# Performance work log

Measured on AMD Instinct MI355X. Metric: run time of the kernel, lower is better.

The kernel has to match this reference:

```python
import math
import jax, jax.numpy as jnp
import numpy as np

D_SCALES = 4  # MSGAD d parameter


def calc_thetas(d):
    # Numeric replication of calculate_theta2 (beta-wavelet polynomial coeffs).
    # p_i(x) = (x/2)^i (1 - x/2)^(d-i) / (2 * Beta(i+1, d+1-i)); keep the d
    # lowest-order coefficients (constant .. x^{d-1}), matching the original.
    thetas = []
    for i in range(d):
        beta = math.factorial(i) * math.factorial(d - i) / math.factorial(d + 1)
        p = (np.poly1d([0.5, 0.0]) ** i) * (np.poly1d([-0.5, 1.0]) ** (d - i)) / (2.0 * beta)
        c = p.coeffs  # highest degree first, length d+1
        thetas.append([float(c[d - j]) for j in range(d)])
    return thetas

THETAS = calc_thetas(D_SCALES)


def setup_inputs() -> dict:
    key = jax.random.key(0)
    k1, k2, k3, k4 = jax.random.split(key, 4)
    N, E, IN, H = 8192, 262144, 256, 128
    in_feat = jax.random.normal(k1, (N, IN), dtype=jnp.float32)
    W = jax.random.normal(k2, (IN, H), dtype=jnp.float32) * 0.05
    b = jnp.zeros((H,), dtype=jnp.float32)
    src = jax.random.randint(k3, (E,), 0, N, dtype=jnp.int32)
    dst = jax.random.randint(k4, (E,), 0, N, dtype=jnp.int32)
    return {"in_feat": in_feat, "W": W, "b": b, "src": src, "dst": dst}


def reference(in_feat, W, b, src, dst):
    N = in_feat.shape[0]
    # Linear + LeakyReLU encoder
    h = jax.nn.leaky_relu(in_feat @ W + b, negative_slope=0.01)
    # dgl.add_self_loop
    loop = jnp.arange(N, dtype=src.dtype)
    s = jnp.concatenate([src, loop])
    d_ = jnp.concatenate([dst, loop])
    # out-degrees (with self loops), D^{-1/2} with clamp(min=1)
    deg = jax.ops.segment_sum(jnp.ones_like(s, dtype=jnp.float32), s, num_segments=N)
    dinv = jnp.maximum(deg, 1.0) ** -0.5  # [N]
    dinv = dinv[:, None]
    outs = []
    for theta in THETAS:
        feat = h
        acc = theta[0] * h
        for k in range(1, len(theta)):
            # unnormalized Laplacian: feat - D^{-1/2} A D^{-1/2} feat
            agg = jax.ops.segment_sum((feat * dinv)[s], d_, num_segments=N)
            feat = feat - agg * dinv
            acc = acc + theta[k] * feat
        outs.append(jnp.einsum('nd,md->nm', acc, acc))  # x @ x.T reconstruction
    return jnp.stack(outs)  # [d, N, N]
```

## Files before the change

kernel.cpp:

```cpp
#include <hip/hip_runtime.h>
#include <hip/hip_bf16.h>

#define N_NODES 8192
#define IN_DIM  256
#define H_DIM   128
#define N_EDGES 262144
#define BI 64
#define BJ 256

typedef __attribute__((ext_vector_type(8))) short bf16x8;
typedef __attribute__((ext_vector_type(4))) float f32x4;
typedef __attribute__((ext_vector_type(4))) short s16x4;

static __device__ inline short bf16_hi(float x) {
    __hip_bfloat16 h = __float2bfloat16(x);
    return *(short*)&h;
}
static __device__ inline float bf16_val(short s) {
    __hip_bfloat16 h = *(__hip_bfloat16*)&s;
    return __bfloat162float(h);
}

__global__ void hist_kernel(const int* __restrict__ src, const int* __restrict__ dst,
                            int* __restrict__ degc, int* __restrict__ dstc) {
    int e = blockIdx.x * 256 + threadIdx.x;
    if (e < N_EDGES) {
        atomicAdd(&degc[src[e]], 1);
        atomicAdd(&dstc[dst[e]], 1);
    }
}

__global__ void scan_kernel(const int* __restrict__ cnt, const int* __restrict__ degc,
                            float* __restrict__ dinv, int* __restrict__ rowptr,
                            int* __restrict__ cursor) {
    __shared__ int buf[2][256];
    int tid = threadIdx.x;
    const int chunk = N_NODES / 256;
    int base = tid * chunk;
    int s = 0;
    for (int i = 0; i < chunk; ++i) {
        s += cnt[base + i];
        dinv[base + i] = 1.0f / sqrtf((float)(degc[base + i] + 1));
    }
    buf[0][tid] = s;
    __syncthreads();
    int pp = 0;
    for (int off = 1; off < 256; off <<= 1) {
        buf[pp ^ 1][tid] = buf[pp][tid] + (tid >= off ? buf[pp][tid - off] : 0);
        pp ^= 1;
        __syncthreads();
    }
    if (tid == 255) rowptr[N_NODES] = buf[pp][255];
    int run = buf[pp][tid] - s;
    for (int i = 0; i < chunk; ++i) {
        rowptr[base + i] = run;
        cursor[base + i] = run;
        run += cnt[base + i];
    }
}

__global__ void fill_kernel(const int* __restrict__ src, const int* __restrict__ dst,
                            int* __restrict__ cursor, int* __restrict__ colidx) {
    int e = blockIdx.x * 256 + threadIdx.x;
    if (e < N_EDGES) {
        int p = atomicAdd(&cursor[dst[e]], 1);
        colidx[p] = src[e];
    }
}

__global__ __launch_bounds__(256) void cvt_kernel(const f32x4* __restrict__ X,
                                                  s16x4* __restrict__ Xhi,
                                                  s16x4* __restrict__ Xlo,
                                                  const float* __restrict__ W,
                                                  short* __restrict__ Wthi,
                                                  short* __restrict__ Wtlo) {
    int blk = blockIdx.x;
    if (blk < 2048) {
        int i = blk * 256 + threadIdx.x;
        f32x4 x = X[i];
        s16x4 hi, lo;
#pragma unroll
        for (int j = 0; j < 4; ++j) {
            short h = bf16_hi(x[j]);
            hi[j] = h;
            lo[j] = bf16_hi(x[j] - bf16_val(h));
        }
        Xhi[i] = hi;
        Xlo[i] = lo;
    } else {
        int t = (blk - 2048) * 256 + threadIdx.x;
        int k = t & 255, j = t >> 8;
        float w = W[k * H_DIM + j];
        short h = bf16_hi(w);
        Wthi[t] = h;
        Wtlo[t] = bf16_hi(w - bf16_val(h));
    }
}

__global__ __launch_bounds__(256) void gemm_h_mfma(const short* __restrict__ Xhi,
                                                   const short* __restrict__ Xlo,
                                                   const short* __restrict__ Wthi,
                                                   const short* __restrict__ Wtlo,
                                                   const float* __restrict__ b,
                                                   float* __restrict__ F0) {
    int lane = threadIdx.x & 63;
    int w    = threadIdx.x >> 6;
    int wr = w >> 1, wc = w & 1;
    int brow = blockIdx.x * 32 + wr * 16;
    int bcol = wc * 64;
    int r16 = lane & 15;
    int kg  = lane >> 4;

    f32x4 c[4] = {};
    for (int kk = 0; kk < IN_DIM / 32; ++kk) {
        int koff = kk * 32 + kg * 8;
        size_t aoff = (size_t)(brow + r16) * IN_DIM + koff;
        bf16x8 ah = *(const bf16x8*)(Xhi + aoff);
        bf16x8 al = *(const bf16x8*)(Xlo + aoff);
        bf16x8 bh[4], bl[4];
#pragma unroll
        for (int n = 0; n < 4; ++n) {
            size_t off = (size_t)(bcol + n * 16 + r16) * IN_DIM + koff;
            bh[n] = *(const bf16x8*)(Wthi + off);
            bl[n] = *(const bf16x8*)(Wtlo + off);
        }
#pragma unroll
        for (int n = 0; n < 4; ++n) {
            c[n] = __builtin_amdgcn_mfma_f32_16x16x32_bf16(ah, bh[n], c[n], 0, 0, 0);
            c[n] = __builtin_amdgcn_mfma_f32_16x16x32_bf16(ah, bl[n], c[n], 0, 0, 0);
            c[n] = __builtin_amdgcn_mfma_f32_16x16x32_bf16(al, bh[n], c[n], 0, 0, 0);
        }
    }
#pragma unroll
    for (int n = 0; n < 4; ++n)
#pragma unroll
        for (int r = 0; r < 4; ++r) {
            int row = brow + kg * 4 + r;
            int col = bcol + n * 16 + r16;
            float v = c[n][r] + b[col];
            v = v > 0.f ? v : 0.01f * v;
            F0[(size_t)row * H_DIM + col] = v;
        }
}

__global__ __launch_bounds__(128) void prop_kernel(const float* __restrict__ Fin,
                                                   float* __restrict__ Fout,
                                                   const float* __restrict__ dinv,
                                                   const int* __restrict__ rowptr,
                                                   const int* __restrict__ colidx) {
    int n = blockIdx.x;
    int j = threadIdx.x;
    float dv  = dinv[n];
    float fs  = Fin[(size_t)n * H_DIM + j];
    float sum = fs * dv;
    int beg = rowptr[n], end = rowptr[n + 1];
    int e = beg;
    for (; e + 4 <= end; e += 4) {
        int s0 = colidx[e], s1 = colidx[e + 1], s2 = colidx[e + 2], s3 = colidx[e + 3];
        float d0 = dinv[s0], d1 = dinv[s1], d2 = dinv[s2], d3 = dinv[s3];
        float v0 = Fin[(size_t)s0 * H_DIM + j];
        float v1 = Fin[(size_t)s1 * H_DIM + j];
        float v2 = Fin[(size_t)s2 * H_DIM + j];
        float v3 = Fin[(size_t)s3 * H_DIM + j];
        sum += v0 * d0 + v1 * d1 + v2 * d2 + v3 * d3;
    }
    for (; e < end; ++e) {
        int s0 = colidx[e];
        sum += Fin[(size_t)s0 * H_DIM + j] * dinv[s0];
    }
    Fout[(size_t)n * H_DIM + j] = fs - sum * dv;
}

__global__ __launch_bounds__(256) void acc_kernel(const f32x4* __restrict__ F0,
                                                  const f32x4* __restrict__ F1,
                                                  const f32x4* __restrict__ F2,
                                                  const f32x4* __restrict__ F3,
                                                  s16x4* __restrict__ accb) {
    int i = blockIdx.x * 256 + threadIdx.x;
    const size_t NH4 = (size_t)N_NODES * H_DIM / 4;
    f32x4 f0 = F0[i], f1 = F1[i], f2 = F2[i], f3 = F3[i];
    f32x4 a0 = 2.5f * f0 - 5.0f * f1 + 3.75f * f2 - 1.25f * f3;
    f32x4 a1 =           5.0f * f1 - 7.5f  * f2 + 3.75f * f3;
    f32x4 a2 =                      3.75f * f2 - 3.75f * f3;
    f32x4 a3 =                                   1.25f * f3;
    s16x4 o0, o1, o2, o3;
#pragma unroll
    for (int j = 0; j < 4; ++j) {
        o0[j] = bf16_hi(a0[j]); o1[j] = bf16_hi(a1[j]);
        o2[j] = bf16_hi(a2[j]); o3[j] = bf16_hi(a3[j]);
    }
    accb[0 * NH4 + i] = o0;
    accb[1 * NH4 + i] = o1;
    accb[2 * NH4 + i] = o2;
    accb[3 * NH4 + i] = o3;
}

__global__ __launch_bounds__(256) void out_gemm_kernel(const short* __restrict__ accb,
                                                       float* __restrict__ out) {
    __shared__ float lds[BI * BJ];
    int jb = blockIdx.x * BJ;
    int ib = blockIdx.y * BI;
    int lane = threadIdx.x & 63;
    int w    = threadIdx.x >> 6;
    int r16 = lane & 15;
    int kg  = lane >> 4;

    for (int t = 0; t < 4; ++t) {
        const short* A = accb + (size_t)t * N_NODES * H_DIM;

        f32x4 c[4][4] = {};
        for (int kk = 0; kk < 4; ++kk) {
            int koff = kk * 32 + kg * 8;
            bf16x8 bi_f[4], aj_f[4];
#pragma unroll
            for (int n = 0; n < 4; ++n)
                bi_f[n] = *(const bf16x8*)(A + (size_t)(ib + n * 16 + r16) * H_DIM + koff);
#pragma unroll
            for (int m = 0; m < 4; ++m)
                aj_f[m] = *(const bf16x8*)(A + (size_t)(jb + w * 64 + m * 16 + r16) * H_DIM + koff);
#pragma unroll
            for (int m = 0; m < 4; ++m)
#pragma unroll
                for (int n = 0; n < 4; ++n)
                    c[m][n] = __builtin_amdgcn_mfma_f32_16x16x32_bf16(aj_f[m], bi_f[n], c[m][n], 0, 0, 0);
        }

        if (t) __syncthreads();
#pragma unroll
        for (int m = 0; m < 4; ++m)
#pragma unroll
            for (int n = 0; n < 4; ++n) {
                int i  = n * 16 + r16;
                int j  = w * 64 + m * 16 + kg * 4;
                int js = j ^ ((i & 7) << 2);
                *(f32x4*)(lds + i * BJ + js) = c[m][n];
            }
        __syncthreads();

        float* O = out + (size_t)t * N_NODES * N_NODES;
#pragma unroll
        for (int p = 0; p < 16; ++p) {
            int r  = p * 4 + w;
            f32x4 v = *(const f32x4*)(lds + r * BJ + lane * 4);
            int jl = (lane * 4) ^ ((r & 7) << 2);
            *(f32x4*)(O + (size_t)(ib + r) * N_NODES + jb + jl) = v;
        }
    }
}

extern "C" void kernel_launch(void* const* d_in, const int* in_sizes, int n_in,
                              void* d_out, int out_size, void* d_ws, size_t ws_size,
                              hipStream_t stream) {
    const float* in_feat = (const float*)d_in[0];
    const float* W       = (const float*)d_in[1];
    const float* b       = (const float*)d_in[2];
    const int*   src     = (const int*)d_in[3];
    const int*   dst     = (const int*)d_in[4];
    float* out = (float*)d_out;

    char* ws = (char*)d_ws;
    const size_t NH4 = (size_t)N_NODES * H_DIM * sizeof(float);
    float* F0 = (float*)(ws + 0 * NH4);
    float* F1 = (float*)(ws + 1 * NH4);
    float* F2 = (float*)(ws + 2 * NH4);
    float* F3 = (float*)(ws + 3 * NH4);
    char*  accb_region = ws + 4 * NH4;
    short* accb = (short*)accb_region;
    short* Xhi = (short*)accb_region;
    short* Xlo = (short*)(accb_region + NH4);
    char* p = ws + 6 * NH4;
    int*   degc   = (int*)p;   p += 32768;
    int*   dstc   = (int*)p;   p += 32768;
    float* dinv   = (float*)p; p += 32768;
    int*   rowptr = (int*)p;   p += 33792;
    int*   cursor = (int*)p;   p += 32768;
    int*   colidx = (int*)p;   p += (size_t)N_EDGES * 4;
    short* Wthi   = (short*)p; p += 65536;
    short* Wtlo   = (short*)p;

    hipMemsetAsync(degc, 0, 65536, stream);

    hist_kernel<<<N_EDGES / 256, 256, 0, stream>>>(src, dst, degc, dstc);
    scan_kernel<<<1, 256, 0, stream>>>(dstc, degc, dinv, rowptr, cursor);
    fill_kernel<<<N_EDGES / 256, 256, 0, stream>>>(src, dst, cursor, colidx);

    cvt_kernel<<<2048 + 128, 256, 0, stream>>>((const f32x4*)in_feat, (s16x4*)Xhi, (s16x4*)Xlo,
                                               W, Wthi, Wtlo);

    gemm_h_mfma<<<N_NODES / 32, 256, 0, stream>>>(Xhi, Xlo, Wthi, Wtlo, b, F0);

    prop_kernel<<<N_NODES, 128, 0, stream>>>(F0, F1, dinv, rowptr, colidx);
    prop_kernel<<<N_NODES, 128, 0, stream>>>(F1, F2, dinv, rowptr, colidx);
    prop_kernel<<<N_NODES, 128, 0, stream>>>(F2, F3, dinv, rowptr, colidx);

    acc_kernel<<<(N_NODES * H_DIM / 4) / 256, 256, 0, stream>>>((const f32x4*)F0, (const f32x4*)F1,
                                                                (const f32x4*)F2, (const f32x4*)F3,
                                                                (s16x4*)accb);

    dim3 g(N_NODES / BJ, N_NODES / BI);
    out_gemm_kernel<<<g, 256, 0, stream>>>(accb, out);
}
```

Before: 408.2 us.

## Prefetch next scale's GEMM fragments during output store in out_gemm

The output GEMM kernel now loads all four k-slices of fragments for the next scale into registers before writing out the current scale's tile from LDS. This lets global loads overlap the large output stores. Full __syncthreads are replaced by raw s_barrier with an explicit lgkmcnt wait, and sched_barriers keep the compiler from reordering. Launch bounds request 2 blocks per CU. The kernel is store-bound on a 1 GB output, and holding the extra fragment registers may limit occupancy.

```diff
diff --git a/kernel.cpp b/kernel.cpp
--- a/kernel.cpp
+++ b/kernel.cpp
@@ -195,8 +195,8 @@
     accb[3 * NH4 + i] = o3;
 }
 
-__global__ __launch_bounds__(256) void out_gemm_kernel(const short* __restrict__ accb,
-                                                       float* __restrict__ out) {
+__global__ __launch_bounds__(256, 2) void out_gemm_kernel(const short* __restrict__ accb,
+                                                          float* __restrict__ out) {
     __shared__ float lds[BI * BJ];
     int jb = blockIdx.x * BJ;
     int ib = blockIdx.y * BI;
@@ -205,27 +205,30 @@
     int r16 = lane & 15;
     int kg  = lane >> 4;
 
+    bf16x8 fA[4][4], fB[4][4];
+#pragma unroll
+    for (int kk = 0; kk < 4; ++kk) {
+        int koff = kk * 32 + kg * 8;
+#pragma unroll
+        for (int n = 0; n < 4; ++n)
+            fB[kk][n] = *(const bf16x8*)(accb + (size_t)(ib + n * 16 + r16) * H_DIM + koff);
+#pragma unroll
+        for (int m = 0; m < 4; ++m)
+            fA[kk][m] = *(const bf16x8*)(accb + (size_t)(jb + w * 64 + m * 16 + r16) * H_DIM + koff);
+    }
+
     for (int t = 0; t < 4; ++t) {
-        const short* A = accb + (size_t)t * N_NODES * H_DIM;
-
         f32x4 c[4][4] = {};
-        for (int kk = 0; kk < 4; ++kk) {
-            int koff = kk * 32 + kg * 8;
-            bf16x8 bi_f[4], aj_f[4];
-#pragma unroll
-            for (int n = 0; n < 4; ++n)
-                bi_f[n] = *(const bf16x8*)(A + (size_t)(ib + n * 16 + r16) * H_DIM + koff);
+#pragma unroll
+        for (int kk = 0; kk < 4; ++kk)
 #pragma unroll
             for (int m = 0; m < 4; ++m)
-                aj_f[m] = *(const bf16x8*)(A + (size_t)(jb + w * 64 + m * 16 + r16) * H_DIM + koff);
-#pragma unroll
-            for (int m = 0; m < 4; ++m)
 #pragma unroll
                 for (int n = 0; n < 4; ++n)
-                    c[m][n] = __builtin_amdgcn_mfma_f32_16x16x32_bf16(aj_f[m], bi_f[n], c[m][n], 0, 0, 0);
-        }
-
-        if (t) __syncthreads();
+                    c[m][n] = __builtin_amdgcn_mfma_f32_16x16x32_bf16(fA[kk][m], fB[kk][n], c[m][n], 0, 0, 0);
+
+        if (t) __builtin_amdgcn_s_barrier();
+
 #pragma unroll
         for (int m = 0; m < 4; ++m)
 #pragma unroll
@@ -235,7 +238,23 @@
                 int js = j ^ ((i & 7) << 2);
                 *(f32x4*)(lds + i * BJ + js) = c[m][n];
             }
-        __syncthreads();
+        asm volatile("s_waitcnt lgkmcnt(0)" ::: "memory");
+        __builtin_amdgcn_s_barrier();
+
+        if (t < 3) {
+            const short* A = accb + (size_t)(t + 1) * N_NODES * H_DIM;
+#pragma unroll
+            for (int kk = 0; kk < 4; ++kk) {
+                int koff = kk * 32 + kg * 8;
+#pragma unroll
+                for (int n = 0; n < 4; ++n)
+                    fB[kk][n] = *(const bf16x8*)(A + (size_t)(ib + n * 16 + r16) * H_DIM + koff);
+#pragma unroll
+                for (int m = 0; m < 4; ++m)
+                    fA[kk][m] = *(const bf16x8*)(A + (size_t)(jb + w * 64 + m * 16 + r16) * H_DIM + koff);
+            }
+        }
+        __builtin_amdgcn_sched_barrier(0);
 
         float* O = out + (size_t)t * N_NODES * N_NODES;
 #pragma unroll
@@ -245,6 +264,7 @@
             int jl = (lane * 4) ^ ((r & 7) << 2);
             *(f32x4*)(O + (size_t)(ib + r) * N_NODES + jb + jl) = v;
         }
+        __builtin_amdgcn_sched_barrier(0);
     }
 }
 
```

After: 432.2 us. 5.9% more time.
